# Performance work log

Measured on AMD Instinct MI355X. Metric: run time of the kernel, lower is better.

## Reference

```python
import jax, jax.numpy as jnp
import numpy as np

NUM_HEADS = 16
EPS = 1e-5


def _layernorm(x, w):
    # torch LayerNorm (biased variance), bias=False
    m = jnp.mean(x, axis=-1, keepdims=True)
    v = jnp.mean(jnp.square(x - m), axis=-1, keepdims=True)
    return (x - m) * jax.lax.rsqrt(v + EPS) * w


def setup_inputs() -> dict:
    key = jax.random.key(0)
    ks = jax.random.split(key, 8)
    B, S, H, A = 2, 2048, 1024, 1024
    hd = H // NUM_HEADS
    return {
        "x": jax.random.normal(ks[0], (B, S, H), jnp.float32),
        "ada_cond": jax.random.normal(ks[1], (B, A), jnp.float32),
        "freqs": jax.random.normal(ks[2], (S, hd // 2, 2), jnp.float32),
        "w_qkv": jax.random.normal(ks[3], (3 * H, H), jnp.float32) * (1.0 / np.sqrt(H)),
        "w_o": jax.random.normal(ks[4], (H, H), jnp.float32) * (1.0 / np.sqrt(H)),
        "ln_w": jnp.ones((H,), jnp.float32),
        "mod_w": jax.random.normal(ks[5], (3 * H, A), jnp.float32) * 0.02,
        "mod_b": jax.random.normal(ks[6], (3 * H,), jnp.float32) * 0.02,
        "qn_w": jnp.ones((hd,), jnp.float32),
        "kn_w": jnp.ones((hd,), jnp.float32),
    }


def reference(x, ada_cond, freqs, w_qkv, w_o, ln_w, mod_w, mod_b, qn_w, kn_w):
    B, S, H = x.shape
    nh = NUM_HEADS
    hd = H // nh

    # pre-norm + AdaLN modulation (with gate)
    h = _layernorm(x, ln_w)
    mod = (jax.nn.silu(ada_cond) @ mod_w.T + mod_b)[:, None, :]  # [B,1,3H]
    scale, shift, gate = jnp.split(mod, 3, axis=-1)
    h = h * (scale + 1.0) + shift

    # QKV projection and head split
    qkv = h @ w_qkv.T                                  # [B,S,3H]
    q, k, v = jnp.split(qkv, 3, axis=-1)
    to_heads = lambda t: t.reshape(B, S, nh, hd).transpose(0, 2, 1, 3)  # [B,nh,S,hd]
    q, k, v = to_heads(q), to_heads(k), to_heads(v)

    # per-head QK layernorm
    q = _layernorm(q, qn_w)
    k = _layernorm(k, kn_w)

    # RoPE (complex rotation via interleaved pairs)
    f = freqs[:S].reshape(1, 1, S, hd // 2, 2)

    def rope(t):
        tr = t.reshape(B, nh, S, hd // 2, 2)
        re = tr[..., 0] * f[..., 0] - tr[..., 1] * f[..., 1]
        im = tr[..., 1] * f[..., 0] + tr[..., 0] * f[..., 1]
        return jnp.stack([re, im], axis=-1).reshape(B, nh, S, hd)

    q, k = rope(q), rope(k)

    # scaled dot-product attention (non-causal)
    scores = jnp.einsum("bhqd,bhkd->bhqk", q, k) * (1.0 / np.sqrt(hd))
    attn = jax.nn.softmax(scores, axis=-1)
    o = jnp.einsum("bhqk,bhkd->bhqd", attn, v)
    o = o.transpose(0, 2, 1, 3).reshape(B, S, H)

    return (o @ w_o.T) * gate
```

## Files before the change

kernel.cpp:

```cpp
#include <hip/hip_runtime.h>
#include <hip/hip_bf16.h>
#include <hip/hip_fp16.h>
#include <math.h>

#define B_ 2
#define S_ 2048
#define H_ 1024
#define A_ 1024
#define NH_ 16
#define HD_ 64
#define H3_ 3072
#define EPS_ 1e-5f

typedef __attribute__((ext_vector_type(8))) short short8;
typedef __attribute__((ext_vector_type(4))) float floatx4;
typedef __attribute__((ext_vector_type(4))) _Float16 half4v;
typedef __attribute__((ext_vector_type(2))) __fp16 fp16x2;

__device__ inline unsigned short f2bf(float x) {
    union { float f; unsigned u; } v; v.f = x;
    unsigned r = v.u + 0x7fffu + ((v.u >> 16) & 1u);
    return (unsigned short)(r >> 16);
}

__device__ inline unsigned pk_bf16(float a, float b) {
    union { __hip_bfloat162 h; unsigned u; } v;
    v.h = __float22bfloat162_rn(make_float2(a, b));
    return v.u;
}

__device__ inline unsigned pk_f16(float a, float b) {
    union { __half2 h; unsigned u; } v;
    v.h = __float22half2_rn(make_float2(a, b));
    return v.u;
}

__device__ inline void gld_lds16(const void* g, void* l) {
    __builtin_amdgcn_global_load_lds(
        (const __attribute__((address_space(1))) unsigned int*)g,
        (__attribute__((address_space(3))) unsigned int*)l, 16, 0, 0);
}

__global__ __launch_bounds__(256) void cast_bf16_kernel(
    const float* __restrict__ in, unsigned short* __restrict__ out, int n)
{
    int i = (blockIdx.x * 256 + threadIdx.x) * 8;
    if (i >= n) return;
    float4 a = *(const float4*)(in + i);
    float4 b = *(const float4*)(in + i + 4);
    uint4 o;
    o.x = pk_bf16(a.x, a.y);
    o.y = pk_bf16(a.z, a.w);
    o.z = pk_bf16(b.x, b.y);
    o.w = pk_bf16(b.z, b.w);
    *(uint4*)(out + i) = o;
}

__global__ __launch_bounds__(256) void mod_gemv_kernel(
    const float* __restrict__ ada, const float* __restrict__ mod_w,
    const float* __restrict__ mod_b, float* __restrict__ mod)
{
    int wid = threadIdx.x >> 6;
    int lane = threadIdx.x & 63;
    int idx = blockIdx.x * 4 + wid;
    int b = idx / H3_;
    int j = idx % H3_;
    const float* ar = ada + (size_t)b * A_;
    const float* wr = mod_w + (size_t)j * A_;
    float acc = 0.f;
    for (int a = lane; a < A_; a += 64) {
        float av = ar[a];
        float sv = av / (1.f + __expf(-av));
        acc += sv * wr[a];
    }
    #pragma unroll
    for (int m = 1; m < 64; m <<= 1) acc += __shfl_xor(acc, m);
    if (lane == 0) mod[idx] = acc + mod_b[j];
}

__global__ __launch_bounds__(256) void ln_mod_kernel(
    const float* __restrict__ x, const float* __restrict__ ln_w,
    const float* __restrict__ mod, unsigned short* __restrict__ hout)
{
    int row = blockIdx.x;
    int b = row >> 11;
    const float* xr = x + (size_t)row * H_;
    int t = threadIdx.x;
    float4 xv = *(const float4*)(xr + t * 4);
    float s1 = xv.x + xv.y + xv.z + xv.w;
    float s2 = xv.x*xv.x + xv.y*xv.y + xv.z*xv.z + xv.w*xv.w;
    #pragma unroll
    for (int m = 1; m < 64; m <<= 1) { s1 += __shfl_xor(s1, m); s2 += __shfl_xor(s2, m); }
    __shared__ float r1[4], r2[4];
    int wid = t >> 6, lane = t & 63;
    if (lane == 0) { r1[wid] = s1; r2[wid] = s2; }
    __syncthreads();
    s1 = r1[0] + r1[1] + r1[2] + r1[3];
    s2 = r2[0] + r2[1] + r2[2] + r2[3];
    float mean = s1 * (1.f / H_);
    float var  = s2 * (1.f / H_) - mean * mean;
    float rstd = rsqrtf(var + EPS_);
    const float* mrow = mod + (size_t)b * H3_;
    float4 wv = *(const float4*)(ln_w + t * 4);
    float4 sc = *(const float4*)(mrow + t * 4);
    float4 sh = *(const float4*)(mrow + H_ + t * 4);
    float4 hv;
    hv.x = (xv.x - mean) * rstd * wv.x * (sc.x + 1.f) + sh.x;
    hv.y = (xv.y - mean) * rstd * wv.y * (sc.y + 1.f) + sh.y;
    hv.z = (xv.z - mean) * rstd * wv.z * (sc.z + 1.f) + sh.z;
    hv.w = (xv.w - mean) * rstd * wv.w * (sc.w + 1.f) + sh.w;
    uint2 o;
    o.x = pk_bf16(hv.x, hv.y);
    o.y = pk_bf16(hv.z, hv.w);
    *(uint2*)(hout + (size_t)row * H_ + t * 4) = o;
}

__global__ __launch_bounds__(256) void gemm_qkv_fused_kernel(
    const unsigned short* __restrict__ A, const unsigned short* __restrict__ Bm,
    const float* __restrict__ freqs, const float* __restrict__ qn_w,
    const float* __restrict__ kn_w, unsigned short* __restrict__ qout,
    unsigned short* __restrict__ kout, unsigned short* __restrict__ vtout)
{
    __shared__ unsigned short As[128 * 32];
    __shared__ unsigned short Bs[128 * 32];
    const int K = H_, N = H3_;
    int t = threadIdx.x;
    int w = t >> 6, lane = t & 63;
    int q16 = lane & 15, quad = lane >> 4;
    int wm = w >> 1, wn = w & 1;
    int m0 = blockIdx.y * 128, n0 = blockIdx.x * 128;

    int srow = (w << 5) + (lane >> 2);
    int soff = (lane & 3) << 3;
    const unsigned short* ga = A + (size_t)(m0 + srow) * K + soff;
    const unsigned short* gb = Bm + (size_t)(n0 + srow) * K + soff;
    unsigned short* la0 = As + (w << 5) * 32;
    unsigned short* la1 = la0 + 16 * 32;
    unsigned short* lb0 = Bs + (w << 5) * 32;
    unsigned short* lb1 = lb0 + 16 * 32;

    floatx4 acc[4][4];
    #pragma unroll
    for (int mt = 0; mt < 4; ++mt)
        #pragma unroll
        for (int nt = 0; nt < 4; ++nt)
            acc[mt][nt] = (floatx4){0.f, 0.f, 0.f, 0.f};

    int a_row = wm * 64 + q16;
    int b_row = wn * 64 + q16;

    for (int kt = 0; kt < K; kt += 32) {
        __syncthreads();
        gld_lds16(ga, la0);
        gld_lds16(ga + (size_t)16 * K, la1);
        gld_lds16(gb, lb0);
        gld_lds16(gb + (size_t)16 * K, lb1);
        ga += 32; gb += 32;
        __syncthreads();

        short8 af[4], bf[4];
        #pragma unroll
        for (int mt = 0; mt < 4; ++mt)
            af[mt] = *(const short8*)&As[(a_row + mt * 16) * 32 + quad * 8];
        #pragma unroll
        for (int nt = 0; nt < 4; ++nt)
            bf[nt] = *(const short8*)&Bs[(b_row + nt * 16) * 32 + quad * 8];
        #pragma unroll
        for (int mt = 0; mt < 4; ++mt)
            #pragma unroll
            for (int nt = 0; nt < 4; ++nt)
                acc[mt][nt] = __builtin_amdgcn_mfma_f32_16x16x32_bf16(
                    af[mt], bf[nt], acc[mt][nt], 0, 0, 0);
    }

    int n_base = n0 + wn * 64;
    int sec = n_base >> 10;
    int head = (n_base & 1023) >> 6;

    if (sec == 2) {
        #pragma unroll
        for (int mt = 0; mt < 4; ++mt) {
            int m = m0 + wm * 64 + mt * 16 + quad * 4;
            int b = m >> 11, s = m & (S_ - 1);
            #pragma unroll
            for (int nt = 0; nt < 4; ++nt) {
                int d = nt * 16 + q16;
                unsigned short* dst =
                    vtout + ((size_t)((b * 16 + head) * 64 + d)) * S_ + s;
                uint2 pk;
                pk.x = pk_f16(acc[mt][nt][0], acc[mt][nt][1]);
                pk.y = pk_f16(acc[mt][nt][2], acc[mt][nt][3]);
                *(uint2*)dst = pk;
            }
        }
    } else {
        const float* nw = (sec == 0) ? qn_w : kn_w;
        float w4[4];
        #pragma unroll
        for (int nt = 0; nt < 4; ++nt) w4[nt] = nw[nt * 16 + q16];
        unsigned short* outp = (sec == 0) ? qout : kout;
        float qscale = (sec == 0) ? 0.1803368801111244f : 1.0f;

        #pragma unroll
        for (int mt = 0; mt < 4; ++mt) {
            #pragma unroll
            for (int i = 0; i < 4; ++i) {
                int m = m0 + wm * 64 + mt * 16 + quad * 4 + i;
                int b = m >> 11, s = m & (S_ - 1);
                float v0 = acc[mt][0][i], v1 = acc[mt][1][i];
                float v2 = acc[mt][2][i], v3 = acc[mt][3][i];
                float s1 = (v0 + v1) + (v2 + v3);
                float s2 = (v0 * v0 + v1 * v1) + (v2 * v2 + v3 * v3);
                #pragma unroll
                for (int msk = 1; msk < 16; msk <<= 1) {
                    s1 += __shfl_xor(s1, msk);
                    s2 += __shfl_xor(s2, msk);
                }
                float mean = s1 * (1.f / 64);
                float var  = s2 * (1.f / 64) - mean * mean;
                float rstd = rsqrtf(var + EPS_);
                float vv[4];
                vv[0] = (v0 - mean) * rstd * w4[0];
                vv[1] = (v1 - mean) * rstd * w4[1];
                vv[2] = (v2 - mean) * rstd * w4[2];
                vv[3] = (v3 - mean) * rstd * w4[3];
                const float* fr = freqs + (size_t)s * 64;
                unsigned short* orow = outp + ((size_t)((b * 16 + head) * S_ + s)) * 64;
                #pragma unroll
                for (int nt = 0; nt < 4; ++nt) {
                    int c = nt * 16 + q16;
                    float vp = __shfl_xor(vv[nt], 1);
                    float2 ff = *(const float2*)(fr + (c & ~1));
                    float r = (c & 1) ? (vv[nt] * ff.x + vp * ff.y)
                                      : (vv[nt] * ff.x - vp * ff.y);
                    orow[c] = f2bf(r * qscale);
                }
            }
        }
    }
}

__global__ __launch_bounds__(256) void gemm_bt_bf16_kernel(
    const unsigned short* __restrict__ A, const unsigned short* __restrict__ Bm,
    float* __restrict__ C, int M, int N, int K,
    const float* __restrict__ gate, int gate_stride, int batch_shift)
{
    __shared__ unsigned short As[128 * 32];
    __shared__ unsigned short Bs[128 * 32];
    int t = threadIdx.x;
    int w = t >> 6, lane = t & 63;
    int q16 = lane & 15, quad = lane >> 4;
    int wm = w >> 1, wn = w & 1;
    int m0 = blockIdx.y * 128, n0 = blockIdx.x * 128;

    int srow = (w << 5) + (lane >> 2);
    int soff = (lane & 3) << 3;
    const unsigned short* ga = A + (size_t)(m0 + srow) * K + soff;
    const unsigned short* gb = Bm + (size_t)(n0 + srow) * K + soff;
    unsigned short* la0 = As + (w << 5) * 32;
    unsigned short* la1 = la0 + 16 * 32;
    unsigned short* lb0 = Bs + (w << 5) * 32;
    unsigned short* lb1 = lb0 + 16 * 32;

    floatx4 acc[4][4];
    #pragma unroll
    for (int mt = 0; mt < 4; ++mt)
        #pragma unroll
        for (int nt = 0; nt < 4; ++nt)
            acc[mt][nt] = (floatx4){0.f, 0.f, 0.f, 0.f};

    int a_row = wm * 64 + q16;
    int b_row = wn * 64 + q16;

    for (int kt = 0; kt < K; kt += 32) {
        __syncthreads();
        gld_lds16(ga, la0);
        gld_lds16(ga + (size_t)16 * K, la1);
        gld_lds16(gb, lb0);
        gld_lds16(gb + (size_t)16 * K, lb1);
        ga += 32; gb += 32;
        __syncthreads();

        short8 af[4], bf[4];
        #pragma unroll
        for (int mt = 0; mt < 4; ++mt)
            af[mt] = *(const short8*)&As[(a_row + mt * 16) * 32 + quad * 8];
        #pragma unroll
        for (int nt = 0; nt < 4; ++nt)
            bf[nt] = *(const short8*)&Bs[(b_row + nt * 16) * 32 + quad * 8];
        #pragma unroll
        for (int mt = 0; mt < 4; ++mt)
            #pragma unroll
            for (int nt = 0; nt < 4; ++nt)
                acc[mt][nt] = __builtin_amdgcn_mfma_f32_16x16x32_bf16(
                    af[mt], bf[nt], acc[mt][nt], 0, 0, 0);
    }

    #pragma unroll
    for (int mt = 0; mt < 4; ++mt) {
        #pragma unroll
        for (int i = 0; i < 4; ++i) {
            int m = m0 + wm * 64 + mt * 16 + quad * 4 + i;
            float* crow = C + (size_t)m * N;
            const float* grow = gate ? gate + (size_t)(m >> batch_shift) * gate_stride
                                     : nullptr;
            #pragma unroll
            for (int nt = 0; nt < 4; ++nt) {
                int n = n0 + wn * 64 + nt * 16 + q16;
                float v = acc[mt][nt][i];
                if (gate) v *= grow[n];
                crow[n] = v;
            }
        }
    }
}

__global__ __launch_bounds__(256, 2) void attn_mfma_kernel(
    const unsigned short* __restrict__ q, const unsigned short* __restrict__ k,
    const unsigned short* __restrict__ vt, unsigned short* __restrict__ o)
{
    __shared__ __align__(16) unsigned char smem[16 * 1024];
    __shared__ float lbuf[4][4][16];
    unsigned short* Vs = (unsigned short*)smem;

    int t = threadIdx.x;
    int w = t >> 6, lane = t & 63;
    int q16 = lane & 15, quad = lane >> 4;
    int bh = blockIdx.y, b = bh >> 4, h = bh & 15;
    int s0 = blockIdx.x * 64;

    const unsigned short* qgp = q + ((size_t)bh * S_ + s0) * HD_;
    short8 qf[4][2];
    #pragma unroll
    for (int qg = 0; qg < 4; ++qg)
        #pragma unroll
        for (int hh = 0; hh < 2; ++hh)
            qf[qg][hh] = *(const short8*)(qgp + (16 * qg + q16) * HD_ + hh * 32 + quad * 8);

    const unsigned short* kg = k + (size_t)bh * S_ * HD_ + (16 * w + q16) * HD_ + quad * 8;

    const unsigned short* vg0 = vt + (size_t)bh * 64 * S_
                              + (size_t)(16 * w + (lane >> 3)) * S_ + (lane & 7) * 8;
    const unsigned short* vg1 = vg0 + 8 * S_;
    unsigned short* vw0 = Vs + (16 * w + (lane >> 3)) * 64 + (((lane & 7) ^ (lane >> 3)) << 3);
    unsigned short* vw1 = vw0 + 512;
    int vroff = q16 * 64 + (((2 * w + (quad >> 1)) ^ (q16 & 7)) << 3) + ((quad & 1) << 2);

    short8 kf_nx0 = *(const short8*)kg;
    short8 kf_nx1 = *(const short8*)(kg + 32);
    uint4 vr0 = *(const uint4*)vg0;
    uint4 vr1 = *(const uint4*)vg1;

    union { half4v h; uint2 u; } ones;
    ones.u.x = 0x3C003C00u; ones.u.y = 0x3C003C00u;

    floatx4 acc_o[4][4];
    floatx4 acc_l[4];
    #pragma unroll
    for (int nd = 0; nd < 4; ++nd)
        #pragma unroll
        for (int qg = 0; qg < 4; ++qg)
            acc_o[nd][qg] = (floatx4){0.f, 0.f, 0.f, 0.f};
    #pragma unroll
    for (int qg = 0; qg < 4; ++qg) acc_l[qg] = (floatx4){0.f, 0.f, 0.f, 0.f};

    for (int kt = 0; kt < S_ / 64; ++kt) {
        short8 kf0 = kf_nx0, kf1 = kf_nx1;
        uint4 v0 = vr0, v1 = vr1;
        __syncthreads();
        *(uint4*)vw0 = v0;
        *(uint4*)vw1 = v1;
        __syncthreads();

        if (kt + 1 < S_ / 64) {
            kg += 64 * HD_; vg0 += 64; vg1 += 64;
            kf_nx0 = *(const short8*)kg;
            kf_nx1 = *(const short8*)(kg + 32);
            vr0 = *(const uint4*)vg0;
            vr1 = *(const uint4*)vg1;
        }

        floatx4 sc[4];
        #pragma unroll
        for (int qg = 0; qg < 4; ++qg) sc[qg] = (floatx4){-12.f, -12.f, -12.f, -12.f};
        #pragma unroll
        for (int qg = 0; qg < 4; ++qg) {
            sc[qg] = __builtin_amdgcn_mfma_f32_16x16x32_bf16(kf0, qf[qg][0], sc[qg], 0, 0, 0);
            sc[qg] = __builtin_amdgcn_mfma_f32_16x16x32_bf16(kf1, qf[qg][1], sc[qg], 0, 0, 0);
        }

        half4v vf[4];
        #pragma unroll
        for (int nd = 0; nd < 4; ++nd)
            vf[nd] = *(const half4v*)&Vs[vroff + nd * 1024];

        #pragma unroll
        for (int qg = 0; qg < 4; ++qg) {
            float p0 = __builtin_amdgcn_exp2f(sc[qg][0]);
            float p1 = __builtin_amdgcn_exp2f(sc[qg][1]);
            float p2 = __builtin_amdgcn_exp2f(sc[qg][2]);
            float p3 = __builtin_amdgcn_exp2f(sc[qg][3]);
            union { half4v h; fp16x2 f2[2]; } pf;
            pf.f2[0] = __builtin_amdgcn_cvt_pkrtz(p0, p1);
            pf.f2[1] = __builtin_amdgcn_cvt_pkrtz(p2, p3);
            acc_l[qg] = __builtin_amdgcn_mfma_f32_16x16x16f16(ones.h, pf.h, acc_l[qg], 0, 0, 0);
            #pragma unroll
            for (int nd = 0; nd < 4; ++nd)
                acc_o[nd][qg] = __builtin_amdgcn_mfma_f32_16x16x16f16(
                    vf[nd], pf.h, acc_o[nd][qg], 0, 0, 0);
        }
    }

    if (quad == 0) {
        #pragma unroll
        for (int qg = 0; qg < 4; ++qg) lbuf[w][qg][q16] = acc_l[qg][0];
    }
    __syncthreads();
    float linv = 1.f / (lbuf[0][w][q16] + lbuf[1][w][q16] + lbuf[2][w][q16] + lbuf[3][w][q16]);

    float* obuf = (float*)smem;
    float* myw = obuf + ((w * 4) * 64 + lane) * 4;
    float* myr = obuf + (w * 64 + lane) * 4;
    unsigned short* og = o + ((size_t)(b * S_ + s0 + 16 * w + q16)) * H_ + h * HD_ + 4 * quad;

    #pragma unroll
    for (int nd = 0; nd < 4; ++nd) {
        __syncthreads();
        #pragma unroll
        for (int qg = 0; qg < 4; ++qg)
            *(floatx4*)(myw + qg * 256) = acc_o[nd][qg];
        __syncthreads();
        floatx4 r0 = *(const floatx4*)(myr);
        floatx4 r1 = *(const floatx4*)(myr + 1024);
        floatx4 r2 = *(const floatx4*)(myr + 2048);
        floatx4 r3 = *(const floatx4*)(myr + 3072);
        floatx4 s = (r0 + r1) + (r2 + r3);
        uint2 pk;
        pk.x = pk_bf16(s[0] * linv, s[1] * linv);
        pk.y = pk_bf16(s[2] * linv, s[3] * linv);
        *(uint2*)(og + nd * 16) = pk;
    }
}

extern "C" void kernel_launch(void* const* d_in, const int* in_sizes, int n_in,
                              void* d_out, int out_size, void* d_ws, size_t ws_size,
                              hipStream_t stream)
{
    const float* x     = (const float*)d_in[0];
    const float* ada   = (const float*)d_in[1];
    const float* freqs = (const float*)d_in[2];
    const float* w_qkv = (const float*)d_in[3];
    const float* w_o   = (const float*)d_in[4];
    const float* ln_w  = (const float*)d_in[5];
    const float* mod_w = (const float*)d_in[6];
    const float* mod_b = (const float*)d_in[7];
    const float* qn_w  = (const float*)d_in[8];
    const float* kn_w  = (const float*)d_in[9];
    float* out = (float*)d_out;

    float* ws  = (float*)d_ws;
    float* mod = ws;
    unsigned short* hb    = (unsigned short*)(mod + 8192);
    unsigned short* qb    = hb + (size_t)B_ * S_ * H_;
    unsigned short* kb    = qb + (size_t)B_ * S_ * H_;
    unsigned short* vtb   = kb + (size_t)B_ * S_ * H_;
    unsigned short* ob    = vtb + (size_t)B_ * S_ * H_;
    unsigned short* wqkvb = ob + (size_t)B_ * S_ * H_;
    unsigned short* wob   = wqkvb + (size_t)H3_ * H_;

    cast_bf16_kernel<<<H3_ * H_ / (8 * 256), 256, 0, stream>>>(w_qkv, wqkvb, H3_ * H_);
    cast_bf16_kernel<<<H_ * H_ / (8 * 256), 256, 0, stream>>>(w_o, wob, H_ * H_);
    mod_gemv_kernel<<<B_ * H3_ / 4, 256, 0, stream>>>(ada, mod_w, mod_b, mod);
    ln_mod_kernel<<<B_ * S_, 256, 0, stream>>>(x, ln_w, mod, hb);
    gemm_qkv_fused_kernel<<<dim3(H3_ / 128, B_ * S_ / 128), 256, 0, stream>>>(
        hb, wqkvb, freqs, qn_w, kn_w, qb, kb, vtb);
    attn_mfma_kernel<<<dim3(S_ / 64, B_ * NH_), 256, 0, stream>>>(qb, kb, vtb, ob);
    gemm_bt_bf16_kernel<<<dim3(H_ / 128, B_ * S_ / 128), 256, 0, stream>>>(
        ob, wob, out, B_ * S_, H_, H_, mod + 2 * H_, H3_, 11);
}
```

Measured before the change: 263.1 us.

## Double GEMM K-tile to 64 with XOR-swizzled LDS and XCD-aware block remap

Both bf16 GEMM kernels now stage 64-wide K slices instead of 32, which halves the number of barrier pairs per output tile. LDS columns are XOR-swizzled by row so the 128-byte-stride fragment reads avoid bank conflicts. Workgroup IDs are remapped so that consecutive tiles group onto the same XCD for better L2 reuse. LDS use per block doubles, which may lower occupancy, and the remap assumes the grid size is a multiple of 8.

Measured after the change: 270.4 us. +2.7%, slower.

```diff
diff --git a/kernel.cpp b/kernel.cpp
--- a/kernel.cpp
+++ b/kernel.cpp
@@ -121,23 +121,25 @@
     const float* __restrict__ kn_w, unsigned short* __restrict__ qout,
     unsigned short* __restrict__ kout, unsigned short* __restrict__ vtout)
 {
-    __shared__ unsigned short As[128 * 32];
-    __shared__ unsigned short Bs[128 * 32];
-    const int K = H_, N = H3_;
+    __shared__ unsigned short As[128 * 64];
+    __shared__ unsigned short Bs[128 * 64];
+    const int K = H_;
     int t = threadIdx.x;
     int w = t >> 6, lane = t & 63;
     int q16 = lane & 15, quad = lane >> 4;
     int wm = w >> 1, wn = w & 1;
-    int m0 = blockIdx.y * 128, n0 = blockIdx.x * 128;
-
-    int srow = (w << 5) + (lane >> 2);
-    int soff = (lane & 3) << 3;
-    const unsigned short* ga = A + (size_t)(m0 + srow) * K + soff;
-    const unsigned short* gb = Bm + (size_t)(n0 + srow) * K + soff;
-    unsigned short* la0 = As + (w << 5) * 32;
-    unsigned short* la1 = la0 + 16 * 32;
-    unsigned short* lb0 = Bs + (w << 5) * 32;
-    unsigned short* lb1 = lb0 + 16 * 32;
+
+    int lin = blockIdx.y * gridDim.x + blockIdx.x;
+    int nwg8 = (gridDim.x * gridDim.y) >> 3;
+    int sb = (lin & 7) * nwg8 + (lin >> 3);
+    int m0 = (sb / gridDim.x) * 128, n0 = (sb % gridDim.x) * 128;
+
+    int srow = (w << 5) + (lane >> 3);
+    int scol = ((lane & 7) ^ (lane >> 3)) << 3;
+    const unsigned short* ga = A + (size_t)(m0 + srow) * K + scol;
+    const unsigned short* gb = Bm + (size_t)(n0 + srow) * K + scol;
+    unsigned short* la = As + (w << 5) * 64;
+    unsigned short* lb = Bs + (w << 5) * 64;
 
     floatx4 acc[4][4];
     #pragma unroll
@@ -148,29 +150,35 @@
 
     int a_row = wm * 64 + q16;
     int b_row = wn * 64 + q16;
-
-    for (int kt = 0; kt < K; kt += 32) {
-        __syncthreads();
-        gld_lds16(ga, la0);
-        gld_lds16(ga + (size_t)16 * K, la1);
-        gld_lds16(gb, lb0);
-        gld_lds16(gb + (size_t)16 * K, lb1);
-        ga += 32; gb += 32;
-        __syncthreads();
-
-        short8 af[4], bf[4];
-        #pragma unroll
-        for (int mt = 0; mt < 4; ++mt)
-            af[mt] = *(const short8*)&As[(a_row + mt * 16) * 32 + quad * 8];
-        #pragma unroll
-        for (int nt = 0; nt < 4; ++nt)
-            bf[nt] = *(const short8*)&Bs[(b_row + nt * 16) * 32 + quad * 8];
-        #pragma unroll
-        for (int mt = 0; mt < 4; ++mt)
+    int swz = (q16 & 7) << 3;
+
+    for (int kt = 0; kt < K; kt += 64) {
+        __syncthreads();
+        #pragma unroll
+        for (int j = 0; j < 4; ++j) {
+            gld_lds16(ga + (size_t)(8 * j) * K, la + (8 * j) * 64);
+            gld_lds16(gb + (size_t)(8 * j) * K, lb + (8 * j) * 64);
+        }
+        ga += 64; gb += 64;
+        __syncthreads();
+
+        #pragma unroll
+        for (int h = 0; h < 2; ++h) {
+            int co = (h * 32 + quad * 8) ^ swz;
+            short8 af[4], bf[4];
+            #pragma unroll
+            for (int mt = 0; mt < 4; ++mt)
+                af[mt] = *(const short8*)&As[(a_row + mt * 16) * 64 + co];
             #pragma unroll
             for (int nt = 0; nt < 4; ++nt)
-                acc[mt][nt] = __builtin_amdgcn_mfma_f32_16x16x32_bf16(
-                    af[mt], bf[nt], acc[mt][nt], 0, 0, 0);
+                bf[nt] = *(const short8*)&Bs[(b_row + nt * 16) * 64 + co];
+            #pragma unroll
+            for (int mt = 0; mt < 4; ++mt)
+                #pragma unroll
+                for (int nt = 0; nt < 4; ++nt)
+                    acc[mt][nt] = __builtin_amdgcn_mfma_f32_16x16x32_bf16(
+                        af[mt], bf[nt], acc[mt][nt], 0, 0, 0);
+        }
     }
 
     int n_base = n0 + wn * 64;
@@ -245,22 +253,24 @@
     float* __restrict__ C, int M, int N, int K,
     const float* __restrict__ gate, int gate_stride, int batch_shift)
 {
-    __shared__ unsigned short As[128 * 32];
-    __shared__ unsigned short Bs[128 * 32];
+    __shared__ unsigned short As[128 * 64];
+    __shared__ unsigned short Bs[128 * 64];
     int t = threadIdx.x;
     int w = t >> 6, lane = t & 63;
     int q16 = lane & 15, quad = lane >> 4;
     int wm = w >> 1, wn = w & 1;
-    int m0 = blockIdx.y * 128, n0 = blockIdx.x * 128;
-
-    int srow = (w << 5) + (lane >> 2);
-    int soff = (lane & 3) << 3;
-    const unsigned short* ga = A + (size_t)(m0 + srow) * K + soff;
-    const unsigned short* gb = Bm + (size_t)(n0 + srow) * K + soff;
-    unsigned short* la0 = As + (w << 5) * 32;
-    unsigned short* la1 = la0 + 16 * 32;
-    unsigned short* lb0 = Bs + (w << 5) * 32;
-    unsigned short* lb1 = lb0 + 16 * 32;
+
+    int lin = blockIdx.y * gridDim.x + blockIdx.x;
+    int nwg8 = (gridDim.x * gridDim.y) >> 3;
+    int sb = (lin & 7) * nwg8 + (lin >> 3);
+    int m0 = (sb / gridDim.x) * 128, n0 = (sb % gridDim.x) * 128;
+
+    int srow = (w << 5) + (lane >> 3);
+    int scol = ((lane & 7) ^ (lane >> 3)) << 3;
+    const unsigned short* ga = A + (size_t)(m0 + srow) * K + scol;
+    const unsigned short* gb = Bm + (size_t)(n0 + srow) * K + scol;
+    unsigned short* la = As + (w << 5) * 64;
+    unsigned short* lb = Bs + (w << 5) * 64;
 
     floatx4 acc[4][4];
     #pragma unroll
@@ -271,29 +281,35 @@
 
     int a_row = wm * 64 + q16;
     int b_row = wn * 64 + q16;
-
-    for (int kt = 0; kt < K; kt += 32) {
-        __syncthreads();
-        gld_lds16(ga, la0);
-        gld_lds16(ga + (size_t)16 * K, la1);
-        gld_lds16(gb, lb0);
-        gld_lds16(gb + (size_t)16 * K, lb1);
-        ga += 32; gb += 32;
-        __syncthreads();
-
-        short8 af[4], bf[4];
-        #pragma unroll
-        for (int mt = 0; mt < 4; ++mt)
-            af[mt] = *(const short8*)&As[(a_row + mt * 16) * 32 + quad * 8];
-        #pragma unroll
-        for (int nt = 0; nt < 4; ++nt)
-            bf[nt] = *(const short8*)&Bs[(b_row + nt * 16) * 32 + quad * 8];
-        #pragma unroll
-        for (int mt = 0; mt < 4; ++mt)
+    int swz = (q16 & 7) << 3;
+
+    for (int kt = 0; kt < K; kt += 64) {
+        __syncthreads();
+        #pragma unroll
+        for (int j = 0; j < 4; ++j) {
+            gld_lds16(ga + (size_t)(8 * j) * K, la + (8 * j) * 64);
+            gld_lds16(gb + (size_t)(8 * j) * K, lb + (8 * j) * 64);
+        }
+        ga += 64; gb += 64;
+        __syncthreads();
+
+        #pragma unroll
+        for (int h = 0; h < 2; ++h) {
+            int co = (h * 32 + quad * 8) ^ swz;
+            short8 af[4], bf[4];
+            #pragma unroll
+            for (int mt = 0; mt < 4; ++mt)
+                af[mt] = *(const short8*)&As[(a_row + mt * 16) * 64 + co];
             #pragma unroll
             for (int nt = 0; nt < 4; ++nt)
-                acc[mt][nt] = __builtin_amdgcn_mfma_f32_16x16x32_bf16(
-                    af[mt], bf[nt], acc[mt][nt], 0, 0, 0);
+                bf[nt] = *(const short8*)&Bs[(b_row + nt * 16) * 64 + co];
+            #pragma unroll
+            for (int mt = 0; mt < 4; ++mt)
+                #pragma unroll
+                for (int nt = 0; nt < 4; ++nt)
+                    acc[mt][nt] = __builtin_amdgcn_mfma_f32_16x16x32_bf16(
+                        af[mt], bf[nt], acc[mt][nt], 0, 0, 0);
+        }
     }
 
     #pragma unroll
```

## Double-buffer LDS tiles and swizzle layout in QKV and output GEMMs

Applied to the files above, without the earlier changes.

Both bf16 GEMM kernels now keep two LDS buffers per operand. The next K-tile's global-to-LDS loads are issued before the MFMAs on the current tile, which cuts one of the two barriers per iteration. The LDS tile is also repacked into 64-element rows with an XOR swizzle, so fragment reads should avoid bank conflicts. LDS use doubles, which may lower occupancy.

Measured after the change: 263.6 us. Within noise of the previous version (+0.2%).

```diff
diff --git a/kernel.cpp b/kernel.cpp
--- a/kernel.cpp
+++ b/kernel.cpp
@@ -40,6 +40,7 @@
         (const __attribute__((address_space(1))) unsigned int*)g,
         (__attribute__((address_space(3))) unsigned int*)l, 16, 0, 0);
 }
+
 
 __global__ __launch_bounds__(256) void cast_bf16_kernel(
     const float* __restrict__ in, unsigned short* __restrict__ out, int n)
@@ -121,23 +122,21 @@
     const float* __restrict__ kn_w, unsigned short* __restrict__ qout,
     unsigned short* __restrict__ kout, unsigned short* __restrict__ vtout)
 {
-    __shared__ unsigned short As[128 * 32];
-    __shared__ unsigned short Bs[128 * 32];
-    const int K = H_, N = H3_;
+    __shared__ unsigned short As[2][128 * 32];
+    __shared__ unsigned short Bs[2][128 * 32];
+    const int K = H_;
     int t = threadIdx.x;
     int w = t >> 6, lane = t & 63;
     int q16 = lane & 15, quad = lane >> 4;
     int wm = w >> 1, wn = w & 1;
     int m0 = blockIdx.y * 128, n0 = blockIdx.x * 128;
 
-    int srow = (w << 5) + (lane >> 2);
-    int soff = (lane & 3) << 3;
-    const unsigned short* ga = A + (size_t)(m0 + srow) * K + soff;
-    const unsigned short* gb = Bm + (size_t)(n0 + srow) * K + soff;
-    unsigned short* la0 = As + (w << 5) * 32;
-    unsigned short* la1 = la0 + 16 * 32;
-    unsigned short* lb0 = Bs + (w << 5) * 32;
-    unsigned short* lb1 = lb0 + 16 * 32;
+    int srow = 2 * (lane >> 3) + ((lane >> 2) & 1);
+    int scol = ((lane & 3) ^ ((lane >> 3) & 3)) << 3;
+    const unsigned short* ga = A + (size_t)(m0 + (w << 5) + srow) * K + scol;
+    const unsigned short* gb = Bm + (size_t)(n0 + (w << 5) + srow) * K + scol;
+    int ldst0 = (w * 16) * 64;
+    int ldst1 = (w * 16 + 8) * 64;
 
     floatx4 acc[4][4];
     #pragma unroll
@@ -146,31 +145,48 @@
         for (int nt = 0; nt < 4; ++nt)
             acc[mt][nt] = (floatx4){0.f, 0.f, 0.f, 0.f};
 
-    int a_row = wm * 64 + q16;
-    int b_row = wn * 64 + q16;
-
-    for (int kt = 0; kt < K; kt += 32) {
-        __syncthreads();
-        gld_lds16(ga, la0);
-        gld_lds16(ga + (size_t)16 * K, la1);
-        gld_lds16(gb, lb0);
-        gld_lds16(gb + (size_t)16 * K, lb1);
-        ga += 32; gb += 32;
-        __syncthreads();
-
+    int abase = (wm * 32 + (q16 >> 1)) * 64 + (q16 & 1) * 32
+              + ((quad ^ ((q16 >> 1) & 3)) << 3);
+    int bbase = (wn * 32 + (q16 >> 1)) * 64 + (q16 & 1) * 32
+              + ((quad ^ ((q16 >> 1) & 3)) << 3);
+
+    gld_lds16(ga, &As[0][ldst0]);
+    gld_lds16(ga + (size_t)16 * K, &As[0][ldst1]);
+    gld_lds16(gb, &Bs[0][ldst0]);
+    gld_lds16(gb + (size_t)16 * K, &Bs[0][ldst1]);
+    __syncthreads();
+
+    int cur = 0;
+    for (int kt = 0; kt < K / 32; ++kt) {
+        const unsigned short* curA = &As[cur][0];
+        const unsigned short* curB = &Bs[cur][0];
         short8 af[4], bf[4];
         #pragma unroll
         for (int mt = 0; mt < 4; ++mt)
-            af[mt] = *(const short8*)&As[(a_row + mt * 16) * 32 + quad * 8];
+            af[mt] = *(const short8*)&curA[abase + mt * 512];
         #pragma unroll
         for (int nt = 0; nt < 4; ++nt)
-            bf[nt] = *(const short8*)&Bs[(b_row + nt * 16) * 32 + quad * 8];
+            bf[nt] = *(const short8*)&curB[bbase + nt * 512];
+
+        if (kt + 1 < K / 32) {
+            const unsigned short* ga2 = ga + (kt + 1) * 32;
+            const unsigned short* gb2 = gb + (kt + 1) * 32;
+            int nb = cur ^ 1;
+            gld_lds16(ga2, &As[nb][ldst0]);
+            gld_lds16(ga2 + (size_t)16 * K, &As[nb][ldst1]);
+            gld_lds16(gb2, &Bs[nb][ldst0]);
+            gld_lds16(gb2 + (size_t)16 * K, &Bs[nb][ldst1]);
+        }
+
         #pragma unroll
         for (int mt = 0; mt < 4; ++mt)
             #pragma unroll
             for (int nt = 0; nt < 4; ++nt)
                 acc[mt][nt] = __builtin_amdgcn_mfma_f32_16x16x32_bf16(
                     af[mt], bf[nt], acc[mt][nt], 0, 0, 0);
+
+        __syncthreads();
+        cur ^= 1;
     }
 
     int n_base = n0 + wn * 64;
@@ -245,22 +261,20 @@
     float* __restrict__ C, int M, int N, int K,
     const float* __restrict__ gate, int gate_stride, int batch_shift)
 {
-    __shared__ unsigned short As[128 * 32];
-    __shared__ unsigned short Bs[128 * 32];
+    __shared__ unsigned short As[2][128 * 32];
+    __shared__ unsigned short Bs[2][128 * 32];
     int t = threadIdx.x;
     int w = t >> 6, lane = t & 63;
     int q16 = lane & 15, quad = lane >> 4;
     int wm = w >> 1, wn = w & 1;
     int m0 = blockIdx.y * 128, n0 = blockIdx.x * 128;
 
-    int srow = (w << 5) + (lane >> 2);
-    int soff = (lane & 3) << 3;
-    const unsigned short* ga = A + (size_t)(m0 + srow) * K + soff;
-    const unsigned short* gb = Bm + (size_t)(n0 + srow) * K + soff;
-    unsigned short* la0 = As + (w << 5) * 32;
-    unsigned short* la1 = la0 + 16 * 32;
-    unsigned short* lb0 = Bs + (w << 5) * 32;
-    unsigned short* lb1 = lb0 + 16 * 32;
+    int srow = 2 * (lane >> 3) + ((lane >> 2) & 1);
+    int scol = ((lane & 3) ^ ((lane >> 3) & 3)) << 3;
+    const unsigned short* ga = A + (size_t)(m0 + (w << 5) + srow) * K + scol;
+    const unsigned short* gb = Bm + (size_t)(n0 + (w << 5) + srow) * K + scol;
+    int ldst0 = (w * 16) * 64;
+    int ldst1 = (w * 16 + 8) * 64;
 
     floatx4 acc[4][4];
     #pragma unroll
@@ -269,31 +283,48 @@
         for (int nt = 0; nt < 4; ++nt)
             acc[mt][nt] = (floatx4){0.f, 0.f, 0.f, 0.f};
 
-    int a_row = wm * 64 + q16;
-    int b_row = wn * 64 + q16;
-
-    for (int kt = 0; kt < K; kt += 32) {
-        __syncthreads();
-        gld_lds16(ga, la0);
-        gld_lds16(ga + (size_t)16 * K, la1);
-        gld_lds16(gb, lb0);
-        gld_lds16(gb + (size_t)16 * K, lb1);
-        ga += 32; gb += 32;
-        __syncthreads();
-
+    int abase = (wm * 32 + (q16 >> 1)) * 64 + (q16 & 1) * 32
+              + ((quad ^ ((q16 >> 1) & 3)) << 3);
+    int bbase = (wn * 32 + (q16 >> 1)) * 64 + (q16 & 1) * 32
+              + ((quad ^ ((q16 >> 1) & 3)) << 3);
+
+    gld_lds16(ga, &As[0][ldst0]);
+    gld_lds16(ga + (size_t)16 * K, &As[0][ldst1]);
+    gld_lds16(gb, &Bs[0][ldst0]);
+    gld_lds16(gb + (size_t)16 * K, &Bs[0][ldst1]);
+    __syncthreads();
+
+    int cur = 0;
+    for (int kt = 0; kt < K / 32; ++kt) {
+        const unsigned short* curA = &As[cur][0];
+        const unsigned short* curB = &Bs[cur][0];
         short8 af[4], bf[4];
         #pragma unroll
         for (int mt = 0; mt < 4; ++mt)
-            af[mt] = *(const short8*)&As[(a_row + mt * 16) * 32 + quad * 8];
+            af[mt] = *(const short8*)&curA[abase + mt * 512];
         #pragma unroll
         for (int nt = 0; nt < 4; ++nt)
-            bf[nt] = *(const short8*)&Bs[(b_row + nt * 16) * 32 + quad * 8];
+            bf[nt] = *(const short8*)&curB[bbase + nt * 512];
+
+        if (kt + 1 < K / 32) {
+            const unsigned short* ga2 = ga + (kt + 1) * 32;
+            const unsigned short* gb2 = gb + (kt + 1) * 32;
+            int nb = cur ^ 1;
+            gld_lds16(ga2, &As[nb][ldst0]);
+            gld_lds16(ga2 + (size_t)16 * K, &As[nb][ldst1]);
+            gld_lds16(gb2, &Bs[nb][ldst0]);
+            gld_lds16(gb2 + (size_t)16 * K, &Bs[nb][ldst1]);
+        }
+
         #pragma unroll
         for (int mt = 0; mt < 4; ++mt)
             #pragma unroll
             for (int nt = 0; nt < 4; ++nt)
                 acc[mt][nt] = __builtin_amdgcn_mfma_f32_16x16x32_bf16(
                     af[mt], bf[nt], acc[mt][nt], 0, 0, 0);
+
+        __syncthreads();
+        cur ^= 1;
     }
 
     #pragma unroll
```
